# Kernel optimization log

Hardware: AMD Instinct MI355X
Metric: run time of the kernel (lower is better)

## Reference

```python
import jax, jax.numpy as jnp
import numpy as np
from jax import lax

HIDDEN = 1024; HEADS = 16; HEAD = 64; LAYERS = 4; MLP = 4096
PATCH = 16; TUBE = 2; CROP = 224; FRAMES = 16
GRID = CROP // PATCH          # 14
DEPTH = FRAMES // TUBE        # 8
N_TOK = DEPTH * GRID * GRID   # 1568
EPS = 1e-6
D_ROT = 2 * ((HEAD // 3) // 2)  # 20 per rotary axis (d, h, w); 4 dims left unrotated


def setup_inputs() -> dict:
    key = jax.random.key(0)
    ks = jax.random.split(key, 12)
    w = lambda k, shape: jax.random.normal(k, shape, jnp.float32) * 0.02
    L, H, M = LAYERS, HIDDEN, MLP
    return {
        "pixel_values_videos": jax.random.normal(ks[0], (2, FRAMES, 3, CROP, CROP), jnp.float32),
        "patch_w": w(ks[1], (H, 3, TUBE, PATCH, PATCH)),  # Conv3d OIDHW
        "patch_b": jnp.zeros((H,), jnp.float32),
        "ln1_g": jnp.ones((L, H), jnp.float32), "ln1_b": jnp.zeros((L, H), jnp.float32),
        "qw": w(ks[2], (L, H, H)), "qb": jnp.zeros((L, H), jnp.float32),
        "kw": w(ks[3], (L, H, H)), "kb": jnp.zeros((L, H), jnp.float32),
        "vw": w(ks[4], (L, H, H)), "vb": jnp.zeros((L, H), jnp.float32),
        "pw": w(ks[5], (L, H, H)), "pb": jnp.zeros((L, H), jnp.float32),
        "ln2_g": jnp.ones((L, H), jnp.float32), "ln2_b": jnp.zeros((L, H), jnp.float32),
        "fc1w": w(ks[6], (L, M, H)), "fc1b": jnp.zeros((L, M), jnp.float32),
        "fc2w": w(ks[7], (L, H, M)), "fc2b": jnp.zeros((L, H), jnp.float32),
        "lnf_g": jnp.ones((H,), jnp.float32), "lnf_b": jnp.zeros((H,), jnp.float32),
    }


def _layer_norm(x, g, b):
    mu = jnp.mean(x, axis=-1, keepdims=True)
    var = jnp.mean(jnp.square(x - mu), axis=-1, keepdims=True)
    return (x - mu) * lax.rsqrt(var + EPS) * g + b


def _position_ids():
    ids = jnp.arange(N_TOK)
    tpf = GRID * GRID
    d_pos = ids // tpf
    rem = ids - d_pos * tpf
    h_pos = rem // GRID
    w_pos = rem - h_pos * GRID
    return d_pos, h_pos, w_pos


def _rotate(x, pos):
    # x: (B, H, N, D); matches VJEPA2 rotate_queries_or_keys:
    # tiled (not interleaved) sin/cos * interleaved rotate-half.
    D = x.shape[-1]
    omega = 1.0 / (10000.0 ** (jnp.arange(D // 2, dtype=x.dtype) / (D / 2.0)))
    freq = pos.astype(x.dtype)[:, None] * omega              # (N, D/2)
    sin = jnp.concatenate([jnp.sin(freq)] * 2, axis=-1)      # (N, D) tiled (torch .repeat)
    cos = jnp.concatenate([jnp.cos(freq)] * 2, axis=-1)
    y = x.reshape(x.shape[:-1] + (D // 2, 2))
    y = jnp.stack([-y[..., 1], y[..., 0]], axis=-1).reshape(x.shape)
    return x * cos + y * sin


def _apply_rope(x, pos_ids):
    d_pos, h_pos, w_pos = pos_ids
    s0, s1, s2 = 0, D_ROT, 2 * D_ROT
    parts = [_rotate(x[..., s0:s1], d_pos), _rotate(x[..., s1:s2], h_pos),
             _rotate(x[..., s2:3 * D_ROT], w_pos)]
    if 3 * D_ROT < HEAD:
        parts.append(x[..., 3 * D_ROT:])
    return jnp.concatenate(parts, axis=-1)


def _forward(pixel_values_videos, patch_w, patch_b, ln1_g, ln1_b, qw, qb, kw, kb,
             vw, vb, pw, pb, ln2_g, ln2_b, fc1w, fc1b, fc2w, fc2b, lnf_g, lnf_b):
    B = pixel_values_videos.shape[0]
    x = jnp.transpose(pixel_values_videos, (0, 2, 1, 3, 4))  # (B, C, T, H, W)
    h = lax.conv_general_dilated(x, patch_w, window_strides=(TUBE, PATCH, PATCH),
                                 padding="VALID",
                                 dimension_numbers=("NCDHW", "OIDHW", "NCDHW"))
    h = h + patch_b[None, :, None, None, None]
    h = h.reshape(B, HIDDEN, -1).transpose(0, 2, 1)          # (B, N, HIDDEN)

    pos_ids = _position_ids()
    scale = HEAD ** -0.5

    for i in range(LAYERS):
        # attention block
        xn = _layer_norm(h, ln1_g[i], ln1_b[i])
        def heads(w_, b_):
            return (xn @ w_.T + b_).reshape(B, N_TOK, HEADS, HEAD).transpose(0, 2, 1, 3)
        q = _apply_rope(heads(qw[i], qb[i]), pos_ids)
        k = _apply_rope(heads(kw[i], kb[i]), pos_ids)
        v = heads(vw[i], vb[i])
        aw = jnp.einsum("bhnd,bhmd->bhnm", q, k) * scale
        aw = jax.nn.softmax(aw.astype(jnp.float32), axis=-1).astype(q.dtype)
        o = jnp.einsum("bhnm,bhmd->bhnd", aw, v)
        o = o.transpose(0, 2, 1, 3).reshape(B, N_TOK, HIDDEN)
        h = h + (o @ pw[i].T + pb[i])
        # MLP block
        xn = _layer_norm(h, ln2_g[i], ln2_b[i])
        m = jax.nn.gelu(xn @ fc1w[i].T + fc1b[i], approximate=False)
        h = h + (m @ fc2w[i].T + fc2b[i])

    return _layer_norm(h, lnf_g, lnf_b)


def reference(pixel_values_videos, patch_w, patch_b, ln1_g, ln1_b, qw, qb, kw, kb,
              vw, vb, pw, pb, ln2_g, ln2_b, fc1w, fc1b, fc2w, fc2b, lnf_g, lnf_b):
    return _forward(pixel_values_videos, patch_w, patch_b, ln1_g, ln1_b, qw, qb, kw, kb,
                    vw, vb, pw, pb, ln2_g, ln2_b, fc1w, fc1b, fc2w, fc2b, lnf_g, lnf_b)
```

## Files before the change

kernel.cpp:

```cpp
#include <hip/hip_runtime.h>
#include <math.h>

#define NTOK   1568
#define BATCH  2
#define HID    1024
#define MLPD   4096
#define NLAYER 4
#define ROWS   (BATCH*NTOK)
#define CONVK  1536

typedef __bf16 bf16x8 __attribute__((ext_vector_type(8)));
typedef __bf16 bf16x2 __attribute__((ext_vector_type(2)));
typedef float  f32x4  __attribute__((ext_vector_type(4)));

__device__ __forceinline__ unsigned short f2b(float f) {
  unsigned int u = __float_as_uint(f);
  unsigned int r = u + 0x7FFFu + ((u >> 16) & 1u);
  return (unsigned short)(r >> 16);
}
__device__ __forceinline__ float b2f(unsigned short s) {
  return __uint_as_float((unsigned int)s << 16);
}
__device__ __forceinline__ unsigned cvt2(float a, float b) {
  bf16x2 t;
  t[0] = (__bf16)a;
  t[1] = (__bf16)b;
  return __builtin_bit_cast(unsigned, t);
}
__device__ __forceinline__ float e2(float x) { return __builtin_amdgcn_exp2f(x); }

__device__ __forceinline__ void async16(const unsigned short* g, unsigned short* l) {
  __builtin_amdgcn_global_load_lds(
      (__attribute__((address_space(1))) void*)(void*)g,
      (__attribute__((address_space(3))) void*)(void*)l, 16, 0, 0);
}

__global__ __launch_bounds__(256) void cast4_k(const float* __restrict__ s,
                                               unsigned short* __restrict__ d,
                                               long long n4) {
  long long i = (long long)blockIdx.x * 256 + threadIdx.x;
  long long stride = (long long)gridDim.x * 256;
  for (; i < n4; i += stride) {
    float4 v = ((const float4*)s)[i];
    *(ushort4*)(d + i * 4) = make_ushort4(f2b(v.x), f2b(v.y), f2b(v.z), f2b(v.w));
  }
}

__global__ __launch_bounds__(256) void castqkv_k(const float* __restrict__ q,
                                                 const float* __restrict__ k,
                                                 const float* __restrict__ v,
                                                 unsigned short* __restrict__ dst) {
  const float* src = blockIdx.y == 0 ? q : (blockIdx.y == 1 ? k : v);
  long long i4 = (long long)blockIdx.x * 256 + threadIdx.x;
  long long e = i4 * 4;
  int layer = (int)(e >> 20);
  long long de = e + ((long long)(2 * layer + blockIdx.y) << 20);
  float4 val = ((const float4*)src)[i4];
  *(ushort4*)(dst + de) = make_ushort4(f2b(val.x), f2b(val.y), f2b(val.z), f2b(val.w));
}

__global__ __launch_bounds__(256) void biascat_k(const float* __restrict__ qb,
                                                 const float* __restrict__ kb,
                                                 const float* __restrict__ vb,
                                                 float* __restrict__ dst) {
  int idx = blockIdx.x * 256 + threadIdx.x;
  int layer = idx / 3072, c = idx % 3072;
  float v = c < 1024 ? qb[layer * 1024 + c]
            : (c < 2048 ? kb[layer * 1024 + c - 1024] : vb[layer * 1024 + c - 2048]);
  dst[idx] = v;
}

__global__ __launch_bounds__(256) void im2col_k(const float* __restrict__ pv,
                                                unsigned short* __restrict__ A) {
  int idx = blockIdx.x * 256 + threadIdx.x;
  int row = idx / CONVK, col = idx % CONVK;
  int b = row / NTOK, t = row % NTOK;
  int d = t / 196, r = t % 196, hh = r / 14, ww = r % 14;
  int c = col >> 9, r2 = col & 511, td = r2 >> 8, ph = (r2 >> 4) & 15, pw = r2 & 15;
  int frame = 2 * d + td;
  const float* src = pv + ((((long long)b * 16 + frame) * 3 + c) * 224 + (hh * 16 + ph)) * 224
                        + (ww * 16 + pw);
  A[idx] = f2b(*src);
}

template <int EPI>
__global__ __launch_bounds__(512, 2) void gemm256(const unsigned short* __restrict__ A,
                                                  const unsigned short* __restrict__ B,
                                                  unsigned short* outP,
                                                  int M, int N, int K, int kChunk,
                                                  size_t zStride,
                                                  const float* __restrict__ bias) {
  __shared__ unsigned short As[4][256 * 32];
  __shared__ unsigned short Bs[4][256 * 32];
  const int tid = threadIdx.x;
  const int lane = tid & 63;
  const int w = tid >> 6;
  const int wr = w >> 2, wc = w & 3;
  const int l15 = lane & 15, l4 = lane >> 4;
  const int wbase = tid & ~63;

  const int gx = gridDim.x, gy = gridDim.y;
  const int nwg = gx * gy * (int)gridDim.z;
  int orig = blockIdx.x + gx * (blockIdx.y + gy * blockIdx.z);
  int q = nwg >> 3, r = nwg & 7, xcd = orig & 7, idx = orig >> 3;
  int swz = (xcd < r ? xcd * (q + 1) : r * (q + 1) + (xcd - r) * q) + idx;
  const int bn = swz % gx;
  int tmp = swz / gx;
  const int bm = tmp % gy;
  const int bz = tmp / gy;
  const int kbeg = bz * kChunk;

  const int r0 = tid >> 2;
  const int g0 = (tid & 3) ^ ((tid >> 3) & 3);
  const int i1 = 512 + tid;
  const int r1 = i1 >> 2;
  const int g1 = (tid & 3) ^ ((i1 >> 3) & 3);
  int ra0 = bm * 256 + r0; if (ra0 >= M) ra0 = M - 1;
  int ra1 = bm * 256 + r1; if (ra1 >= M) ra1 = M - 1;
  const int rb0 = bn * 256 + r0;
  const int rb1 = bn * 256 + r1;
  const size_t Ao0 = (size_t)ra0 * K + g0 * 8;
  const size_t Ao1 = (size_t)ra1 * K + g1 * 8;
  const size_t Bo0 = (size_t)rb0 * K + g0 * 8;
  const size_t Bo1 = (size_t)rb1 * K + g1 * 8;

  auto stA = [&](int buf, int k0) {
    async16(A + Ao0 + k0, &As[buf][wbase * 8]);
    async16(A + Ao1 + k0, &As[buf][4096 + wbase * 8]);
  };
  auto stB = [&](int buf, int k0) {
    async16(B + Bo0 + k0, &Bs[buf][wbase * 8]);
    async16(B + Bo1 + k0, &Bs[buf][4096 + wbase * 8]);
  };

  f32x4 acc[8][4] = {};
  const int nk = kChunk >> 5;

  stA(0, kbeg); stB(0, kbeg);
  stA(1, kbeg + 32); stB(1, kbeg + 32);
  stA(2, kbeg + 64); stB(2, kbeg + 64);

  const int pchunk = (l4 ^ ((l15 >> 1) & 3)) * 8;
  const int abase = (wr * 128 + l15) * 32 + pchunk;
  const int bbase = (wc * 64 + l15) * 32 + pchunk;

  for (int kt = 0; kt < nk; ++kt) {
    if (kt < nk - 2) {
      asm volatile("s_waitcnt vmcnt(8)" ::: "memory");
    } else if (kt == nk - 2) {
      asm volatile("s_waitcnt vmcnt(4)" ::: "memory");
    } else {
      asm volatile("s_waitcnt vmcnt(0)" ::: "memory");
    }
    __builtin_amdgcn_s_barrier();
    __builtin_amdgcn_sched_barrier(0);
    const int cur = kt & 3;
    const int pre = (kt + 3) & 3;
    const bool doPre = (kt + 3 < nk);
    const int kpre = kbeg + (kt + 3) * 32;

    if (doPre) stA(pre, kpre);
    bf16x8 bfr[4], af[4];
#pragma unroll
    for (int n = 0; n < 4; ++n)
      bfr[n] = *(const bf16x8*)&Bs[cur][bbase + n * 512];
#pragma unroll
    for (int m = 0; m < 4; ++m)
      af[m] = *(const bf16x8*)&As[cur][abase + m * 512];
    __builtin_amdgcn_s_setprio(1);
#pragma unroll
    for (int m = 0; m < 4; ++m)
#pragma unroll
      for (int n = 0; n < 4; ++n)
        acc[m][n] = __builtin_amdgcn_mfma_f32_16x16x32_bf16(af[m], bfr[n], acc[m][n], 0, 0, 0);
    __builtin_amdgcn_s_setprio(0);

    if (doPre) stB(pre, kpre);
#pragma unroll
    for (int m = 0; m < 4; ++m)
      af[m] = *(const bf16x8*)&As[cur][abase + (m + 4) * 512];
    __builtin_amdgcn_s_setprio(1);
#pragma unroll
    for (int m = 0; m < 4; ++m)
#pragma unroll
      for (int n = 0; n < 4; ++n)
        acc[m + 4][n] = __builtin_amdgcn_mfma_f32_16x16x32_bf16(af[m], bfr[n], acc[m + 4][n], 0, 0, 0);
    __builtin_amdgcn_s_setprio(0);
  }

  float bsv[4] = {0, 0, 0, 0};
  if (EPI >= 1) {
#pragma unroll
    for (int n = 0; n < 4; ++n)
      bsv[n] = bias[bn * 256 + wc * 64 + n * 16 + l15];
  }
  unsigned short* pout = outP + (size_t)bz * zStride;
#pragma unroll
  for (int m = 0; m < 8; ++m) {
    int rowb = bm * 256 + wr * 128 + m * 16 + l4 * 4;
#pragma unroll
    for (int rr2 = 0; rr2 < 4; ++rr2) {
      int rr = rowb + rr2;
      if (rr >= M) continue;
#pragma unroll
      for (int n = 0; n < 4; ++n) {
        int col = bn * 256 + wc * 64 + n * 16 + l15;
        float v = acc[m][n][rr2];
        if (EPI >= 1) v += bsv[n];
        if (EPI == 2) v = 0.5f * v * (1.0f + erff(v * 0.70710678118654752f));
        pout[(size_t)rr * N + col] = f2b(v);
      }
    }
  }
}

template <int NP, int RESID, int FINAL>
__global__ __launch_bounds__(256) void redln_k(const unsigned short* __restrict__ p,
                                               const float* __restrict__ bias,
                                               const float* resid,
                                               const float* __restrict__ g,
                                               const float* __restrict__ b,
                                               float* hOut,
                                               unsigned short* __restrict__ xnOut,
                                               float* __restrict__ fOut,
                                               size_t pStride) {
  __shared__ float red[8];
  const int row = blockIdx.x, tid = threadIdx.x;
  const int col = tid * 4;
  const size_t off = (size_t)row * HID + col;
  float v0 = 0, v1 = 0, v2 = 0, v3 = 0;
#pragma unroll
  for (int pp = 0; pp < NP; ++pp) {
    ushort4 a = *(const ushort4*)(p + (size_t)pp * pStride + off);
    v0 += b2f(a.x); v1 += b2f(a.y); v2 += b2f(a.z); v3 += b2f(a.w);
  }
  float4 bs = *(const float4*)(bias + col);
  v0 += bs.x; v1 += bs.y; v2 += bs.z; v3 += bs.w;
  if (RESID) {
    float4 r = *(const float4*)(resid + off);
    v0 += r.x; v1 += r.y; v2 += r.z; v3 += r.w;
  }
  if (!FINAL) *(float4*)(hOut + off) = make_float4(v0, v1, v2, v3);
  float s = v0 + v1 + v2 + v3;
  float q = v0 * v0 + v1 * v1 + v2 * v2 + v3 * v3;
  for (int o2 = 32; o2; o2 >>= 1) { s += __shfl_xor(s, o2); q += __shfl_xor(q, o2); }
  if ((tid & 63) == 0) { red[tid >> 6] = s; red[4 + (tid >> 6)] = q; }
  __syncthreads();
  float ts = red[0] + red[1] + red[2] + red[3];
  float tq = red[4] + red[5] + red[6] + red[7];
  float mu = ts * (1.0f / HID);
  float var = tq * (1.0f / HID) - mu * mu;
  float rs = rsqrtf(var + 1e-6f);
  float o0 = (v0 - mu) * rs * g[col + 0] + b[col + 0];
  float o1 = (v1 - mu) * rs * g[col + 1] + b[col + 1];
  float o2 = (v2 - mu) * rs * g[col + 2] + b[col + 2];
  float o3 = (v3 - mu) * rs * g[col + 3] + b[col + 3];
  if (FINAL) {
    *(float4*)(fOut + off) = make_float4(o0, o1, o2, o3);
  } else {
    *(ushort4*)(xnOut + off) = make_ushort4(f2b(o0), f2b(o1), f2b(o2), f2b(o3));
  }
}

__global__ __launch_bounds__(256) void qkvprep_k(const unsigned short* __restrict__ qkvb,
                                                 unsigned short* __restrict__ Qh,
                                                 unsigned short* __restrict__ Kh,
                                                 unsigned short* __restrict__ VT) {
  __shared__ unsigned short Vs[64 * 72];
  const int tile = blockIdx.x, bh = blockIdx.y;
  const int b = bh >> 4, head = bh & 15;
  const int tid = threadIdx.x;
  const int tl = tid >> 2, dc = tid & 3;
  const int tg = tile * 64 + tl;
  const int trc = tg < NTOK ? tg : NTOK - 1;
  const bool valid = tg < NTOK;
  const size_t srow = ((size_t)(b * NTOK + trc)) * 3072 + head * 64 + dc * 16;

  {
    uint4 v0 = *(const uint4*)(qkvb + srow + 2048);
    uint4 v1 = *(const uint4*)(qkvb + srow + 2048 + 8);
    *(uint4*)&Vs[tl * 72 + dc * 16] = v0;
    *(uint4*)&Vs[tl * 72 + dc * 16 + 8] = v1;
  }

  const int t = trc;
  const int dpos = t / 196, rem = t - dpos * 196, hpos = rem / 14, wpos = rem - hpos * 14;
  const float LG = 0.9210340371976184f;
  union V16 { uint4 u[2]; unsigned short s[16]; };
  V16 qin, kin, qout, kout;
  qin.u[0] = *(const uint4*)(qkvb + srow);
  qin.u[1] = *(const uint4*)(qkvb + srow + 8);
  kin.u[0] = *(const uint4*)(qkvb + srow + 1024);
  kin.u[1] = *(const uint4*)(qkvb + srow + 1024 + 8);
#pragma unroll
  for (int p = 0; p < 8; ++p) {
    int d0 = dc * 16 + 2 * p;
    float qx0 = b2f(qin.s[2 * p]), qx1 = b2f(qin.s[2 * p + 1]);
    float kx0 = b2f(kin.s[2 * p]), kx1 = b2f(kin.s[2 * p + 1]);
    float qo0, qo1, ko0, ko1;
    if (d0 >= 60) { qo0 = qx0; qo1 = qx1; ko0 = kx0; ko1 = kx1; }
    else {
      int region = d0 / 20;
      int j0 = d0 - region * 20;
      int pos = region == 0 ? dpos : (region == 1 ? hpos : wpos);
      float fp = (float)pos;
      int i0 = j0 % 10, i1 = (j0 + 1) % 10;
      float f0 = expf(-LG * (float)i0) * fp;
      float f1 = expf(-LG * (float)i1) * fp;
      float c0 = cosf(f0), s0 = sinf(f0), c1 = cosf(f1), s1 = sinf(f1);
      qo0 = qx0 * c0 - qx1 * s0; qo1 = qx1 * c1 + qx0 * s1;
      ko0 = kx0 * c0 - kx1 * s0; ko1 = kx1 * c1 + kx0 * s1;
    }
    const float QS = 0.18033688011112042f;
    qout.s[2 * p]     = f2b(qo0 * QS);
    qout.s[2 * p + 1] = f2b(qo1 * QS);
    kout.s[2 * p]     = f2b(ko0);
    kout.s[2 * p + 1] = f2b(ko1);
  }
  if (valid) {
    size_t drow = ((size_t)bh * NTOK + tg) * 64 + dc * 16;
    *(uint4*)(Qh + drow)     = qout.u[0];
    *(uint4*)(Qh + drow + 8) = qout.u[1];
    *(uint4*)(Kh + drow)     = kout.u[0];
    *(uint4*)(Kh + drow + 8) = kout.u[1];
  }
  __syncthreads();
  {
    int d = tid >> 2, tc = tid & 3;
    if (tile * 64 + tc * 16 < NTOK) {
      V16 o;
#pragma unroll
      for (int jj = 0; jj < 16; ++jj) o.s[jj] = Vs[(tc * 16 + jj) * 72 + d];
      unsigned short* dst = VT + ((size_t)bh * 64 + d) * NTOK + tile * 64 + tc * 16;
      *(uint4*)dst = o.u[0];
      *(uint4*)(dst + 8) = o.u[1];
    }
  }
}

#define SM_BLOCK(S, MREG, LREG, OACC, PF)                                        \
  {                                                                              \
    float rmax = S[0][0];                                                        \
    _Pragma("unroll") for (int nt = 0; nt < 4; ++nt)                             \
      _Pragma("unroll") for (int rr = 0; rr < 4; ++rr)                           \
        rmax = fmaxf(rmax, S[nt][rr]);                                           \
    rmax = fmaxf(rmax, __shfl_xor(rmax, 16));                                    \
    rmax = fmaxf(rmax, __shfl_xor(rmax, 32));                                    \
    if (!__all(rmax - MREG <= 11.5f)) {                                          \
      float mn = fmaxf(MREG, rmax);                                              \
      float alpha = e2(MREG - mn);                                               \
      MREG = mn;                                                                 \
      LREG *= alpha;                                                             \
      _Pragma("unroll") for (int dt = 0; dt < 4; ++dt)                           \
        _Pragma("unroll") for (int rr = 0; rr < 4; ++rr) OACC[dt][rr] *= alpha;  \
    }                                                                            \
    float rsum = 0.0f;                                                           \
    _Pragma("unroll") for (int nt = 0; nt < 4; ++nt)                             \
      _Pragma("unroll") for (int rr = 0; rr < 4; ++rr) {                         \
        float pv = e2(S[nt][rr] - MREG);                                         \
        S[nt][rr] = pv;                                                          \
        rsum += pv;                                                              \
      }                                                                          \
    rsum += __shfl_xor(rsum, 16);                                                \
    rsum += __shfl_xor(rsum, 32);                                                \
    LREG += rsum;                                                                \
    unsigned pk01[4], pk23[4];                                                   \
    _Pragma("unroll") for (int nt = 0; nt < 4; ++nt) {                           \
      pk01[nt] = cvt2(S[nt][0], S[nt][1]);                                       \
      pk23[nt] = cvt2(S[nt][2], S[nt][3]);                                       \
    }                                                                            \
    _Pragma("unroll") for (int kc = 0; kc < 2; ++kc) {                           \
      unsigned t0, t1;                                                           \
      t0 = __shfl(pk01[2 * kc], srcA); t1 = __shfl(pk01[2 * kc + 1], srcA);      \
      PF[kc].u[0] = hi ? t1 : t0;                                                \
      t0 = __shfl(pk23[2 * kc], srcA); t1 = __shfl(pk23[2 * kc + 1], srcA);      \
      PF[kc].u[1] = hi ? t1 : t0;                                                \
      t0 = __shfl(pk01[2 * kc], srcB); t1 = __shfl(pk01[2 * kc + 1], srcB);      \
      PF[kc].u[2] = hi ? t1 : t0;                                                \
      t0 = __shfl(pk23[2 * kc], srcB); t1 = __shfl(pk23[2 * kc + 1], srcB);      \
      PF[kc].u[3] = hi ? t1 : t0;                                                \
    }                                                                            \
  }

__global__ __launch_bounds__(256, 3) void flash6_k(const unsigned short* __restrict__ Qh,
                                                   const unsigned short* __restrict__ Kh,
                                                   const unsigned short* __restrict__ VT,
                                                   unsigned short* __restrict__ Opart,
                                                   float2* __restrict__ ml) {
  __shared__ unsigned short Ks[3][64 * 64];
  __shared__ unsigned short Vs[3][64 * 64];
  const int bh = blockIdx.x, qt = blockIdx.y, kv = blockIdx.z;
  const int kt0 = kv ? 13 : 0, kt1 = kv ? 25 : 13;
  const int tid = threadIdx.x, lane = tid & 63, w = tid >> 6;
  const int l15 = lane & 15, l4 = lane >> 4;
  const size_t hb = (size_t)bh * NTOK * 64;
  const unsigned short* kgp = Kh + hb;
  const unsigned short* vbp = VT + (size_t)bh * 64 * NTOK;

  const int srow0 = w * 8 + (lane >> 3);
  const int scg0  = (lane & 7) ^ (srow0 & 7);
  const int srow1 = srow0 + 32;
  const int scg1  = (lane & 7) ^ (srow1 & 7);

  auto stage = [&](int buf, int kc) {
    async16(kgp + (size_t)(kc + srow0) * 64 + scg0 * 8, &Ks[buf][(size_t)w * 512]);
    async16(kgp + (size_t)(kc + srow1) * 64 + scg1 * 8, &Ks[buf][(size_t)(w + 4) * 512]);
    async16(vbp + (size_t)srow0 * NTOK + kc + scg0 * 8, &Vs[buf][(size_t)w * 512]);
    async16(vbp + (size_t)srow1 * NTOK + kc + scg1 * 8, &Vs[buf][(size_t)(w + 4) * 512]);
  };

  const int qrow0 = qt * 128 + w * 32 + l15;
  const int qrow1 = qrow0 + 16;
  const int qrc0 = qrow0 < NTOK ? qrow0 : NTOK - 1;
  const int qrc1 = qrow1 < NTOK ? qrow1 : NTOK - 1;
  bf16x8 qa0 = *(const bf16x8*)(Qh + hb + (size_t)qrc0 * 64 + l4 * 8);
  bf16x8 qa1 = *(const bf16x8*)(Qh + hb + (size_t)qrc0 * 64 + 32 + l4 * 8);
  bf16x8 qb0 = *(const bf16x8*)(Qh + hb + (size_t)qrc1 * 64 + l4 * 8);
  bf16x8 qb1 = *(const bf16x8*)(Qh + hb + (size_t)qrc1 * 64 + 32 + l4 * 8);

  f32x4 oaccA[4] = {}, oaccB[4] = {};
  float mA = -1e30f, lA = 0.0f, mB = -1e30f, lB = 0.0f;

  stage(0, kt0 * 64);
  stage(1, (kt0 + 1) * 64);

  const int h7 = l15 & 7;
  const int p1 = (l4 ^ h7) * 8;
  const int p2 = ((l4 + 4) ^ h7) * 8;
  const int srcA = ((l4 & 1) << 5) | l15;
  const int srcB = srcA + 16;
  const bool hi = (l4 >> 1) != 0;

  int cur = 0;
  for (int kt = kt0; kt < kt1; ++kt) {
    const int kb = kt * 64;
    if (kt + 1 < kt1) {
      asm volatile("s_waitcnt vmcnt(4)" ::: "memory");
    } else {
      asm volatile("s_waitcnt vmcnt(0)" ::: "memory");
    }
    __builtin_amdgcn_s_barrier();
    __builtin_amdgcn_sched_barrier(0);
    if (kt + 2 < kt1) {
      int nxt2 = cur + 2; if (nxt2 >= 3) nxt2 -= 3;
      stage(nxt2, (kt + 2) * 64);
    }

    bf16x8 kc0[4], kc1[4];
#pragma unroll
    for (int nt = 0; nt < 4; ++nt) {
      const unsigned short* kr = &Ks[cur][(nt * 16 + l15) * 64];
      kc0[nt] = *(const bf16x8*)(kr + p1);
      kc1[nt] = *(const bf16x8*)(kr + p2);
    }
    f32x4 sA[4] = {}, sB[4] = {};
    __builtin_amdgcn_s_setprio(1);
#pragma unroll
    for (int nt = 0; nt < 4; ++nt) {
      sA[nt] = __builtin_amdgcn_mfma_f32_16x16x32_bf16(kc0[nt], qa0, sA[nt], 0, 0, 0);
      sA[nt] = __builtin_amdgcn_mfma_f32_16x16x32_bf16(kc1[nt], qa1, sA[nt], 0, 0, 0);
      sB[nt] = __builtin_amdgcn_mfma_f32_16x16x32_bf16(kc0[nt], qb0, sB[nt], 0, 0, 0);
      sB[nt] = __builtin_amdgcn_mfma_f32_16x16x32_bf16(kc1[nt], qb1, sB[nt], 0, 0, 0);
    }
    __builtin_amdgcn_s_setprio(0);
    bf16x8 vf0[4], vf1[4];
#pragma unroll
    for (int dt = 0; dt < 4; ++dt) {
      const unsigned short* vr = &Vs[cur][(dt * 16 + l15) * 64];
      vf0[dt] = *(const bf16x8*)(vr + p1);
      vf1[dt] = *(const bf16x8*)(vr + p2);
    }

    if (kb + 64 > NTOK) {
#pragma unroll
      for (int nt = 0; nt < 4; ++nt)
#pragma unroll
        for (int rr = 0; rr < 4; ++rr)
          if (kb + nt * 16 + l4 * 4 + rr >= NTOK) { sA[nt][rr] = -1e30f; sB[nt][rr] = -1e30f; }
    }

    union PB { unsigned u[4]; bf16x8 v; } pfA[2], pfB[2];
    SM_BLOCK(sA, mA, lA, oaccA, pfA)
    __builtin_amdgcn_s_setprio(1);
#pragma unroll
    for (int dt = 0; dt < 4; ++dt) {
      oaccA[dt] = __builtin_amdgcn_mfma_f32_16x16x32_bf16(vf0[dt], pfA[0].v, oaccA[dt], 0, 0, 0);
      oaccA[dt] = __builtin_amdgcn_mfma_f32_16x16x32_bf16(vf1[dt], pfA[1].v, oaccA[dt], 0, 0, 0);
    }
    __builtin_amdgcn_s_setprio(0);
    SM_BLOCK(sB, mB, lB, oaccB, pfB)
    __builtin_amdgcn_s_setprio(1);
#pragma unroll
    for (int dt = 0; dt < 4; ++dt) {
      oaccB[dt] = __builtin_amdgcn_mfma_f32_16x16x32_bf16(vf0[dt], pfB[0].v, oaccB[dt], 0, 0, 0);
      oaccB[dt] = __builtin_amdgcn_mfma_f32_16x16x32_bf16(vf1[dt], pfB[1].v, oaccB[dt], 0, 0, 0);
    }
    __builtin_amdgcn_s_setprio(0);
    cur = cur + 1 == 3 ? 0 : cur + 1;
  }

  __syncthreads();
  unsigned short* Os = &Ks[0][0];
#pragma unroll
  for (int dt = 0; dt < 4; ++dt)
#pragma unroll
    for (int rr = 0; rr < 4; ++rr)
      Os[w * 1152 + l15 * 72 + dt * 16 + l4 * 4 + rr] = f2b(oaccA[dt][rr]);
  if (qrow0 < NTOK) {
    uint4 a  = *(const uint4*)&Os[w * 1152 + l15 * 72 + l4 * 16];
    uint4 bq = *(const uint4*)&Os[w * 1152 + l15 * 72 + l4 * 16 + 8];
    unsigned short* op = Opart + ((size_t)(kv * 32 + bh) * NTOK + qrow0) * 64;
    *(uint4*)(op + l4 * 16) = a;
    *(uint4*)(op + l4 * 16 + 8) = bq;
    if (l4 == 0) ml[(size_t)(kv * 32 + bh) * NTOK + qrow0] = make_float2(mA, lA);
  }
  __builtin_amdgcn_sched_barrier(0);
#pragma unroll
  for (int dt = 0; dt < 4; ++dt)
#pragma unroll
    for (int rr = 0; rr < 4; ++rr)
      Os[w * 1152 + l15 * 72 + dt * 16 + l4 * 4 + rr] = f2b(oaccB[dt][rr]);
  if (qrow1 < NTOK) {
    uint4 a  = *(const uint4*)&Os[w * 1152 + l15 * 72 + l4 * 16];
    uint4 bq = *(const uint4*)&Os[w * 1152 + l15 * 72 + l4 * 16 + 8];
    unsigned short* op = Opart + ((size_t)(kv * 32 + bh) * NTOK + qrow1) * 64;
    *(uint4*)(op + l4 * 16) = a;
    *(uint4*)(op + l4 * 16 + 8) = bq;
    if (l4 == 0) ml[(size_t)(kv * 32 + bh) * NTOK + qrow1] = make_float2(mB, lB);
  }
}

__global__ __launch_bounds__(256) void fcomb_k(const unsigned short* __restrict__ Op,
                                               const float2* __restrict__ ml,
                                               unsigned short* __restrict__ O) {
  const int bh = blockIdx.x, qt = blockIdx.y;
  const int tid = threadIdx.x;
  const int qr = qt * 64 + (tid >> 2);
  const int dc = (tid & 3) * 16;
  if (qr >= NTOK) return;
  const int b = bh >> 4, head = bh & 15;
  float2 a0 = ml[(size_t)bh * NTOK + qr];
  float2 a1 = ml[(size_t)(32 + bh) * NTOK + qr];
  float M = fmaxf(a0.x, a1.x);
  float w0 = e2(a0.x - M), w1 = e2(a1.x - M);
  float inv = 1.0f / (a0.y * w0 + a1.y * w1);
  w0 *= inv; w1 *= inv;
  union V16 { uint4 u[2]; unsigned short s[16]; } p0, p1, o;
  const unsigned short* q0 = Op + ((size_t)bh * NTOK + qr) * 64 + dc;
  const unsigned short* q1 = Op + ((size_t)(32 + bh) * NTOK + qr) * 64 + dc;
  p0.u[0] = *(const uint4*)q0;       p0.u[1] = *(const uint4*)(q0 + 8);
  p1.u[0] = *(const uint4*)q1;       p1.u[1] = *(const uint4*)(q1 + 8);
#pragma unroll
  for (int j = 0; j < 16; ++j) o.s[j] = f2b(b2f(p0.s[j]) * w0 + b2f(p1.s[j]) * w1);
  unsigned short* dst = O + ((size_t)(b * NTOK + qr)) * HID + head * 64 + dc;
  *(uint4*)dst = o.u[0];
  *(uint4*)(dst + 8) = o.u[1];
}

extern "C" void kernel_launch(void* const* d_in, const int* in_sizes, int n_in,
                              void* d_out, int out_size, void* d_ws, size_t ws_size,
                              hipStream_t stream) {
  (void)in_sizes; (void)n_in; (void)out_size; (void)ws_size;
  const float* pv      = (const float*)d_in[0];
  const float* patch_w = (const float*)d_in[1];
  const float* patch_b = (const float*)d_in[2];
  const float* ln1_g   = (const float*)d_in[3];
  const float* ln1_b   = (const float*)d_in[4];
  const float* qw = (const float*)d_in[5];
  const float* qb = (const float*)d_in[6];
  const float* kw = (const float*)d_in[7];
  const float* kb = (const float*)d_in[8];
  const float* vw = (const float*)d_in[9];
  const float* vb = (const float*)d_in[10];
  const float* pw = (const float*)d_in[11];
  const float* pb = (const float*)d_in[12];
  const float* ln2_g = (const float*)d_in[13];
  const float* ln2_b = (const float*)d_in[14];
  const float* fc1w = (const float*)d_in[15];
  const float* fc1b = (const float*)d_in[16];
  const float* fc2w = (const float*)d_in[17];
  const float* fc2b = (const float*)d_in[18];
  const float* lnf_g = (const float*)d_in[19];
  const float* lnf_b = (const float*)d_in[20];

  char* wsp = (char*)d_ws;
  auto alloc = [&](size_t bytes) {
    char* p = wsp;
    wsp += (bytes + 255) & ~(size_t)255;
    return p;
  };
  unsigned short* wPatch = (unsigned short*)alloc((size_t)1024 * 1536 * 2);
  unsigned short* wQKV   = (unsigned short*)alloc((size_t)NLAYER * 3072 * 1024 * 2);
  unsigned short* wP     = (unsigned short*)alloc((size_t)NLAYER * HID * HID * 2);
  unsigned short* wF1    = (unsigned short*)alloc((size_t)NLAYER * MLPD * HID * 2);
  unsigned short* wF2    = (unsigned short*)alloc((size_t)NLAYER * HID * MLPD * 2);
  float*          qkvbias = (float*)alloc((size_t)NLAYER * 3072 * 4);
  unsigned short* Aim  = (unsigned short*)alloc((size_t)ROWS * CONVK * 2);
  float*          h    = (float*)alloc((size_t)ROWS * HID * 4);
  unsigned short* xnb  = (unsigned short*)alloc((size_t)ROWS * HID * 2);
  unsigned short* qkvo = (unsigned short*)alloc((size_t)ROWS * 3072 * 2);
  unsigned short* Qh   = (unsigned short*)alloc((size_t)ROWS * HID * 2 + 8192);
  unsigned short* Kh   = (unsigned short*)alloc((size_t)ROWS * HID * 2 + 8192);
  unsigned short* VT   = (unsigned short*)alloc((size_t)ROWS * HID * 2 + 8192);
  unsigned short* ob   = (unsigned short*)alloc((size_t)ROWS * HID * 2);
  unsigned short* mb   = (unsigned short*)alloc((size_t)ROWS * MLPD * 2);

  unsigned short* part  = Qh;
  unsigned short* partM = mb;
  unsigned short* Opart = mb;
  float2*         mlbuf = (float2*)(mb + (size_t)2 * 32 * NTOK * 64);
  const size_t MNs = (size_t)ROWS * HID;

  auto cast = [&](const float* s, unsigned short* d, long long n) {
    long long n4 = n / 4;
    int grid = (int)((n4 + 255) / 256);
    if (grid > 16384) grid = 16384;
    cast4_k<<<grid, 256, 0, stream>>>(s, d, n4);
  };
  cast(patch_w, wPatch, (long long)1024 * 1536);
  castqkv_k<<<dim3(4096, 3), 256, 0, stream>>>(qw, kw, vw, wQKV);
  cast(pw, wP, (long long)NLAYER * HID * HID);
  cast(fc1w, wF1, (long long)NLAYER * MLPD * HID);
  cast(fc2w, wF2, (long long)NLAYER * HID * MLPD);
  biascat_k<<<48, 256, 0, stream>>>(qb, kb, vb, qkvbias);

  im2col_k<<<(ROWS * CONVK) / 256, 256, 0, stream>>>(pv, Aim);
  gemm256<0><<<dim3(4, 13, 4), 512, 0, stream>>>(
      Aim, wPatch, part, ROWS, HID, CONVK, 384, MNs, nullptr);
  redln_k<4, 0, 0><<<ROWS, 256, 0, stream>>>(
      part, patch_b, nullptr, ln1_g, ln1_b, h, xnb, nullptr, MNs);

  for (int i = 0; i < NLAYER; ++i) {
    gemm256<1><<<dim3(12, 13, 1), 512, 0, stream>>>(
        xnb, wQKV + (size_t)i * 3072 * 1024, qkvo, ROWS, 3072, HID, 1024,
        0, qkvbias + i * 3072);
    qkvprep_k<<<dim3(25, 32), 256, 0, stream>>>(qkvo, Qh, Kh, VT);
    flash6_k<<<dim3(32, 13, 2), 256, 0, stream>>>(Qh, Kh, VT, Opart, mlbuf);
    fcomb_k<<<dim3(32, 25), 256, 0, stream>>>(Opart, mlbuf, ob);
    gemm256<0><<<dim3(4, 13, 4), 512, 0, stream>>>(
        ob, wP + (size_t)i * HID * HID, partM, ROWS, HID, HID, 256, MNs, nullptr);
    redln_k<4, 1, 0><<<ROWS, 256, 0, stream>>>(
        partM, pb + i * HID, h, ln2_g + i * HID, ln2_b + i * HID, h, xnb, nullptr, MNs);
    gemm256<2><<<dim3(16, 13, 1), 512, 0, stream>>>(
        xnb, wF1 + (size_t)i * MLPD * HID, mb, ROWS, MLPD, HID, 1024,
        0, fc1b + i * MLPD);
    gemm256<0><<<dim3(4, 13, 4), 512, 0, stream>>>(
        mb, wF2 + (size_t)i * HID * MLPD, part, ROWS, HID, MLPD, 1024, MNs, nullptr);
    if (i < NLAYER - 1) {
      redln_k<4, 1, 0><<<ROWS, 256, 0, stream>>>(
          part, fc2b + i * HID, h, ln1_g + (i + 1) * HID, ln1_b + (i + 1) * HID,
          h, xnb, nullptr, MNs);
    } else {
      redln_k<4, 1, 1><<<ROWS, 256, 0, stream>>>(
          part, fc2b + i * HID, h, lnf_g, lnf_b, nullptr, nullptr, (float*)d_out, MNs);
    }
  }
}
```

Measured before the change: 1.320 ms.

## Restructure GEMM mainloop to BK=64 double buffer with quadrant-interleaved loads

Switches the 256x256 bf16 GEMM from a 4-stage BK=32 ring buffer to a 2-stage BK=64 double buffer. Each k-step is split into four MFMA quadrants, with half-tile async global->LDS loads for the next stage placed between them. A new XOR swizzle over 8 chunks keeps LDS reads conflict-free. The goal is fewer barriers per unit of K and finer overlap of loads with MFMA. The cost is a shallower prefetch depth and more barriers inside each iteration, so memory latency may be hidden less well.

```diff
diff --git a/kernel.cpp b/kernel.cpp
--- a/kernel.cpp
+++ b/kernel.cpp
@@ -90,14 +90,13 @@
                                                   int M, int N, int K, int kChunk,
                                                   size_t zStride,
                                                   const float* __restrict__ bias) {
-  __shared__ unsigned short As[4][256 * 32];
-  __shared__ unsigned short Bs[4][256 * 32];
+  __shared__ unsigned short As[2][256 * 64];
+  __shared__ unsigned short Bs[2][256 * 64];
   const int tid = threadIdx.x;
   const int lane = tid & 63;
   const int w = tid >> 6;
   const int wr = w >> 2, wc = w & 3;
   const int l15 = lane & 15, l4 = lane >> 4;
-  const int wbase = tid & ~63;
 
   const int gx = gridDim.x, gy = gridDim.y;
   const int nwg = gx * gy * (int)gridDim.z;
@@ -110,101 +109,152 @@
   const int bz = tmp / gy;
   const int kbeg = bz * kChunk;
 
-  const int r0 = tid >> 2;
-  const int g0 = (tid & 3) ^ ((tid >> 3) & 3);
-  const int i1 = 512 + tid;
-  const int r1 = i1 >> 2;
-  const int g1 = (tid & 3) ^ ((i1 >> 3) & 3);
-  int ra0 = bm * 256 + r0; if (ra0 >= M) ra0 = M - 1;
-  int ra1 = bm * 256 + r1; if (ra1 >= M) ra1 = M - 1;
-  const int rb0 = bn * 256 + r0;
-  const int rb1 = bn * 256 + r1;
-  const size_t Ao0 = (size_t)ra0 * K + g0 * 8;
-  const size_t Ao1 = (size_t)ra1 * K + g1 * 8;
-  const size_t Bo0 = (size_t)rb0 * K + g0 * 8;
-  const size_t Bo1 = (size_t)rb1 * K + g1 * 8;
-
-  auto stA = [&](int buf, int k0) {
-    async16(A + Ao0 + k0, &As[buf][wbase * 8]);
-    async16(A + Ao1 + k0, &As[buf][4096 + wbase * 8]);
+  const int r5 = tid >> 3;
+  const int gc8 = ((tid & 7) ^ (r5 & 7)) * 8;
+  int ar0 = bm * 256 + r5;        if (ar0 >= M) ar0 = M - 1;
+  int ar1 = bm * 256 + 64 + r5;   if (ar1 >= M) ar1 = M - 1;
+  int ar2 = bm * 256 + 128 + r5;  if (ar2 >= M) ar2 = M - 1;
+  int ar3 = bm * 256 + 192 + r5;  if (ar3 >= M) ar3 = M - 1;
+  const size_t Ao0 = (size_t)ar0 * K + gc8;
+  const size_t Ao1 = (size_t)ar1 * K + gc8;
+  const size_t Ao2 = (size_t)ar2 * K + gc8;
+  const size_t Ao3 = (size_t)ar3 * K + gc8;
+  const int aw8 = w * 512;
+  const int q5 = r5 >> 5, r31 = r5 & 31;
+  const size_t Bo00 = (size_t)(bn * 256 +       q5 * 64 +      r31) * K + gc8;
+  const size_t Bo01 = (size_t)(bn * 256 + 128 + q5 * 64 +      r31) * K + gc8;
+  const size_t Bo10 = (size_t)(bn * 256 +       q5 * 64 + 32 + r31) * K + gc8;
+  const size_t Bo11 = (size_t)(bn * 256 + 128 + q5 * 64 + 32 + r31) * K + gc8;
+  const int bwrow = (w >> 2) * 64 + 8 * (w & 3);
+  const int bl00 = (bwrow) * 64;
+  const int bl01 = (128 + bwrow) * 64;
+  const int bl10 = (32 + bwrow) * 64;
+  const int bl11 = (160 + bwrow) * 64;
+
+  auto stAh = [&](int bf, int h, int k0) {
+    if (h == 0) {
+      async16(A + Ao0 + k0, &As[bf][aw8]);
+      async16(A + Ao2 + k0, &As[bf][2 * 4096 + aw8]);
+    } else {
+      async16(A + Ao1 + k0, &As[bf][1 * 4096 + aw8]);
+      async16(A + Ao3 + k0, &As[bf][3 * 4096 + aw8]);
+    }
   };
-  auto stB = [&](int buf, int k0) {
-    async16(B + Bo0 + k0, &Bs[buf][wbase * 8]);
-    async16(B + Bo1 + k0, &Bs[buf][4096 + wbase * 8]);
+  auto stBh = [&](int bf, int nh, int k0) {
+    if (nh == 0) {
+      async16(B + Bo00 + k0, &Bs[bf][bl00]);
+      async16(B + Bo01 + k0, &Bs[bf][bl01]);
+    } else {
+      async16(B + Bo10 + k0, &Bs[bf][bl10]);
+      async16(B + Bo11 + k0, &Bs[bf][bl11]);
+    }
   };
 
   f32x4 acc[8][4] = {};
-  const int nk = kChunk >> 5;
-
-  stA(0, kbeg); stB(0, kbeg);
-  stA(1, kbeg + 32); stB(1, kbeg + 32);
-  stA(2, kbeg + 64); stB(2, kbeg + 64);
-
-  const int pchunk = (l4 ^ ((l15 >> 1) & 3)) * 8;
-  const int abase = (wr * 128 + l15) * 32 + pchunk;
-  const int bbase = (wc * 64 + l15) * 32 + pchunk;
+  const int nk = kChunk >> 6;
+
+  const int h7 = l15 & 7;
+  const int pc0 = (l4 ^ h7) * 8;
+  const int pc1 = ((l4 + 4) ^ h7) * 8;
+  const int abase = (wr * 128 + l15) * 64;
+  const int bbase = (wc * 64 + l15) * 64;
+
+#define READ_A(MH)                                                                 \
+  _Pragma("unroll")                                                                \
+  for (int mm = 0; mm < 4; ++mm) {                                                 \
+    afr[mm][0] = *(const bf16x8*)&As[cur][abase + ((MH) * 64 + mm * 16) * 64 + pc0]; \
+    afr[mm][1] = *(const bf16x8*)&As[cur][abase + ((MH) * 64 + mm * 16) * 64 + pc1]; \
+  }
+#define READ_B(NH)                                                                 \
+  _Pragma("unroll")                                                                \
+  for (int nn = 0; nn < 2; ++nn) {                                                 \
+    bfr[NH][nn][0] = *(const bf16x8*)&Bs[cur][bbase + ((NH) * 32 + nn * 16) * 64 + pc0]; \
+    bfr[NH][nn][1] = *(const bf16x8*)&Bs[cur][bbase + ((NH) * 32 + nn * 16) * 64 + pc1]; \
+  }
+#define QUAD(MH, NH)                                                               \
+  _Pragma("unroll")                                                                \
+  for (int mm = 0; mm < 4; ++mm) {                                                 \
+    _Pragma("unroll")                                                              \
+    for (int nn = 0; nn < 2; ++nn) {                                               \
+      acc[(MH)*4+mm][(NH)*2+nn] = __builtin_amdgcn_mfma_f32_16x16x32_bf16(         \
+          afr[mm][0], bfr[NH][nn][0], acc[(MH)*4+mm][(NH)*2+nn], 0, 0, 0);         \
+      acc[(MH)*4+mm][(NH)*2+nn] = __builtin_amdgcn_mfma_f32_16x16x32_bf16(         \
+          afr[mm][1], bfr[NH][nn][1], acc[(MH)*4+mm][(NH)*2+nn], 0, 0, 0);         \
+    }                                                                              \
+  }
+
+  stAh(0, 0, kbeg); stBh(0, 0, kbeg); stBh(0, 1, kbeg); stAh(0, 1, kbeg);
+  asm volatile("s_waitcnt vmcnt(4)" ::: "memory");
+  __builtin_amdgcn_s_barrier();
+  __builtin_amdgcn_sched_barrier(0);
 
   for (int kt = 0; kt < nk; ++kt) {
-    if (kt < nk - 2) {
-      asm volatile("s_waitcnt vmcnt(8)" ::: "memory");
-    } else if (kt == nk - 2) {
-      asm volatile("s_waitcnt vmcnt(4)" ::: "memory");
-    } else {
-      asm volatile("s_waitcnt vmcnt(0)" ::: "memory");
-    }
+    const int cur = kt & 1, nxt = cur ^ 1;
+    const bool st = (kt + 1 < nk);
+    const int kn = kbeg + (kt + 1) * 64;
+    bf16x8 afr[4][2], bfr[2][2][2];
+
+    READ_A(0)
+    READ_B(0)
+    if (st) stAh(nxt, 0, kn);
+    __builtin_amdgcn_s_barrier();
+    __builtin_amdgcn_s_setprio(1);
+    QUAD(0, 0)
+    __builtin_amdgcn_s_setprio(0);
+    if (st) { asm volatile("s_waitcnt vmcnt(4)" ::: "memory"); }
+    else    { asm volatile("s_waitcnt vmcnt(2)" ::: "memory"); }
     __builtin_amdgcn_s_barrier();
     __builtin_amdgcn_sched_barrier(0);
-    const int cur = kt & 3;
-    const int pre = (kt + 3) & 3;
-    const bool doPre = (kt + 3 < nk);
-    const int kpre = kbeg + (kt + 3) * 32;
-
-    if (doPre) stA(pre, kpre);
-    bf16x8 bfr[4], af[4];
-#pragma unroll
-    for (int n = 0; n < 4; ++n)
-      bfr[n] = *(const bf16x8*)&Bs[cur][bbase + n * 512];
-#pragma unroll
-    for (int m = 0; m < 4; ++m)
-      af[m] = *(const bf16x8*)&As[cur][abase + m * 512];
+
+    READ_B(1)
+    if (st) stBh(nxt, 0, kn);
+    __builtin_amdgcn_s_barrier();
     __builtin_amdgcn_s_setprio(1);
-#pragma unroll
-    for (int m = 0; m < 4; ++m)
-#pragma unroll
-      for (int n = 0; n < 4; ++n)
-        acc[m][n] = __builtin_amdgcn_mfma_f32_16x16x32_bf16(af[m], bfr[n], acc[m][n], 0, 0, 0);
+    QUAD(0, 1)
     __builtin_amdgcn_s_setprio(0);
-
-    if (doPre) stB(pre, kpre);
-#pragma unroll
-    for (int m = 0; m < 4; ++m)
-      af[m] = *(const bf16x8*)&As[cur][abase + (m + 4) * 512];
+    if (st) { asm volatile("s_waitcnt vmcnt(4)" ::: "memory"); }
+    else    { asm volatile("s_waitcnt vmcnt(0)" ::: "memory"); }
+    __builtin_amdgcn_s_barrier();
+    __builtin_amdgcn_sched_barrier(0);
+
+    READ_A(1)
+    if (st) stBh(nxt, 1, kn);
+    __builtin_amdgcn_s_barrier();
     __builtin_amdgcn_s_setprio(1);
-#pragma unroll
-    for (int m = 0; m < 4; ++m)
-#pragma unroll
-      for (int n = 0; n < 4; ++n)
-        acc[m + 4][n] = __builtin_amdgcn_mfma_f32_16x16x32_bf16(af[m], bfr[n], acc[m + 4][n], 0, 0, 0);
+    QUAD(1, 1)
     __builtin_amdgcn_s_setprio(0);
-  }
+    __builtin_amdgcn_s_barrier();
+
+    if (st) stAh(nxt, 1, kn);
+    __builtin_amdgcn_s_barrier();
+    __builtin_amdgcn_s_setprio(1);
+    QUAD(1, 0)
+    __builtin_amdgcn_s_setprio(0);
+    if (st) { asm volatile("s_waitcnt vmcnt(4)" ::: "memory"); }
+    __builtin_amdgcn_s_barrier();
+    __builtin_amdgcn_sched_barrier(0);
+  }
+#undef READ_A
+#undef READ_B
+#undef QUAD
 
   float bsv[4] = {0, 0, 0, 0};
   if (EPI >= 1) {
 #pragma unroll
     for (int n = 0; n < 4; ++n)
-      bsv[n] = bias[bn * 256 + wc * 64 + n * 16 + l15];
+      bsv[n] = bias[bn * 256 + wc * 64 + (n >> 1) * 32 + (n & 1) * 16 + l15];
   }
   unsigned short* pout = outP + (size_t)bz * zStride;
 #pragma unroll
   for (int m = 0; m < 8; ++m) {
-    int rowb = bm * 256 + wr * 128 + m * 16 + l4 * 4;
+    int rowb = bm * 256 + wr * 128 + (m >> 2) * 64 + (m & 3) * 16 + l4 * 4;
 #pragma unroll
     for (int rr2 = 0; rr2 < 4; ++rr2) {
       int rr = rowb + rr2;
       if (rr >= M) continue;
 #pragma unroll
       for (int n = 0; n < 4; ++n) {
-        int col = bn * 256 + wc * 64 + n * 16 + l15;
+        int col = bn * 256 + wc * 64 + (n >> 1) * 32 + (n & 1) * 16 + l15;
         float v = acc[m][n][rr2];
         if (EPI >= 1) v += bsv[n];
         if (EPI == 2) v = 0.5f * v * (1.0f + erff(v * 0.70710678118654752f));
```

Measured after the change: 1.274 ms. -3.5%, faster.
